# Optimization experiments

Measured on AMD Instinct MI355X. Metric: run time of the kernel, lower is better.

The kernel has to match this reference:

```python
import jax, jax.numpy as jnp
import numpy as np

B, NINP, NCLS = 16384, 2048, 100


def setup_inputs() -> dict:
    key = jax.random.key(0)
    k1, k2, k3, k4, k5 = jax.random.split(key, 5)
    s = 1.0 / np.sqrt(NINP)
    return {
        "time_series": jax.random.normal(k1, (B, NINP), jnp.float32),
        "w_weight": jax.random.uniform(k2, (NINP, NINP), jnp.float32, -s, s),
        "w_bias": jax.random.uniform(k3, (NINP,), jnp.float32, -s, s),
        "fc_weight": jax.random.uniform(k4, (NCLS, NINP), jnp.float32, -s, s),
        "fc_bias": jax.random.uniform(k5, (NCLS,), jnp.float32, -s, s),
    }


def reference(time_series, w_weight, w_bias, fc_weight, fc_bias):
    # time_series: [B, N]
    n = time_series.shape[1]
    # gamma = cumsum(softmax(w(x), axis=1), axis=1): monotone warp in (0, 1]
    gamma = jnp.cumsum(jax.nn.softmax(time_series @ w_weight.T + w_bias, axis=1), axis=1)
    # Interp1d(linspace(0,1,N), x, gamma): per-row linear interpolation,
    # sampling each series at the warped time points gamma.
    xs = jnp.linspace(0.0, 1.0, n, dtype=time_series.dtype)  # shared knot grid
    warped = jax.vmap(lambda g, y: jnp.interp(g, xs, y))(gamma, time_series)  # [B, N]
    return warped @ fc_weight.T + fc_bias  # [B, nclasses]
```

## Files before the change

kernel.cpp:

```cpp
#include <hip/hip_runtime.h>
#include <hip/hip_bf16.h>

#define BROWS 16384
#define NDIM  2048
#define NCLS  100

typedef __attribute__((ext_vector_type(8))) __bf16 bf16x8;
typedef __attribute__((ext_vector_type(4))) float f32x4;
typedef __attribute__((ext_vector_type(16))) float f32x16;
typedef __attribute__((ext_vector_type(4))) unsigned short u16x4;
typedef __attribute__((ext_vector_type(8))) unsigned short u16x8;

__device__ __forceinline__ unsigned short f2bf(float f) {
    union { float f; unsigned int u; } v; v.f = f;
    unsigned int u = v.u;
    unsigned int r = (u + 0x7fffu + ((u >> 16) & 1u)) >> 16;
    return (unsigned short)r;
}
__device__ __forceinline__ float bf2f(unsigned short h) {
    union { unsigned int u; float f; } v; v.u = ((unsigned int)h) << 16;
    return v.f;
}

#define GLOAD_LDS(g, l) \
    __builtin_amdgcn_global_load_lds((const __attribute__((address_space(1))) void*)(g), \
                                     (__attribute__((address_space(3))) void*)(l), 16, 0, 0)

__global__ __launch_bounds__(256) void prep_kernel(const float4* __restrict__ x,
                                                   const float4* __restrict__ w,
                                                   u16x4* __restrict__ xhi, u16x4* __restrict__ xlo,
                                                   u16x4* __restrict__ whi, u16x4* __restrict__ wlo,
                                                   int n4x, int n4w)
{
    int i = blockIdx.x * 256 + threadIdx.x;
    const float4* src; u16x4 *hi, *lo; int idx;
    if (i < n4x) { src = x; hi = xhi; lo = xlo; idx = i; }
    else { idx = i - n4x; if (idx >= n4w) return; src = w; hi = whi; lo = wlo; }
    float4 v = src[idx];
    u16x4 h, l;
    h.x = f2bf(v.x); l.x = f2bf(v.x - bf2f(h.x));
    h.y = f2bf(v.y); l.y = f2bf(v.y - bf2f(h.y));
    h.z = f2bf(v.z); l.z = f2bf(v.z - bf2f(h.z));
    h.w = f2bf(v.w); l.w = f2bf(v.w - bf2f(h.w));
    hi[idx] = h; lo[idx] = l;
}

__global__ __launch_bounds__(256) void cvt_bf16_kernel(const float4* __restrict__ src,
                                                       u16x4* __restrict__ dst, int n4)
{
    int i = blockIdx.x * 256 + threadIdx.x;
    if (i >= n4) return;
    float4 v = src[i];
    u16x4 h;
    h.x = f2bf(v.x); h.y = f2bf(v.y); h.z = f2bf(v.z); h.w = f2bf(v.w);
    dst[i] = h;
}

__global__ __launch_bounds__(256) void gemm1_mfma_fused_kernel(
        const unsigned short* __restrict__ xhi,
        const unsigned short* __restrict__ xlo,
        const unsigned short* __restrict__ whi,
        const unsigned short* __restrict__ wlo,
        const float* __restrict__ bias,
        float* __restrict__ C)
{
    __shared__ unsigned short sAh[128 * 32];
    __shared__ unsigned short sAl[128 * 32];
    __shared__ unsigned short sBh[128 * 32];
    __shared__ unsigned short sBl[128 * 32];

    const int tid  = threadIdx.x;
    const int lane = tid & 63;
    const int w    = tid >> 6;
    const int wm   = w & 1;
    const int wn   = w >> 1;
    const int m0   = blockIdx.y * 128;
    const int n0   = blockIdx.x * 128;

    const int c0 = w * 128 + lane;
    const int r0 = c0 >> 2;
    const int q0 = (c0 & 3) ^ ((r0 >> 1) & 3);
    const int c1 = c0 + 64;
    const int r1 = c1 >> 2;
    const int q1 = (c1 & 3) ^ ((r1 >> 1) & 3);

    const size_t a_goff0 = (size_t)(m0 + r0) * NDIM + q0 * 8;
    const size_t a_goff1 = (size_t)(m0 + r1) * NDIM + q1 * 8;
    const size_t b_goff0 = (size_t)(n0 + r0) * NDIM + q0 * 8;
    const size_t b_goff1 = (size_t)(n0 + r1) * NDIM + q1 * 8;

    unsigned short* ldsAh0 = &sAh[w * 1024];   unsigned short* ldsAh1 = &sAh[w * 1024 + 512];
    unsigned short* ldsAl0 = &sAl[w * 1024];   unsigned short* ldsAl1 = &sAl[w * 1024 + 512];
    unsigned short* ldsBh0 = &sBh[w * 1024];   unsigned short* ldsBh1 = &sBh[w * 1024 + 512];
    unsigned short* ldsBl0 = &sBl[w * 1024];   unsigned short* ldsBl1 = &sBl[w * 1024 + 512];

    const int ln32 = lane & 31;
    const int lk2  = lane >> 5;
    int offA[2][2], offB[2][2];
#pragma unroll
    for (int i = 0; i < 2; i++) {
#pragma unroll
        for (int ks = 0; ks < 2; ks++) {
            int ra = wm * 64 + i * 32 + ln32;
            offA[i][ks] = ra * 32 + (((2 * ks + lk2) ^ ((ra >> 1) & 3)) * 8);
            int rb = wn * 64 + i * 32 + ln32;
            offB[i][ks] = rb * 32 + (((2 * ks + lk2) ^ ((rb >> 1) & 3)) * 8);
        }
    }

    f32x16 acc[2][2];
#pragma unroll
    for (int i = 0; i < 2; i++)
#pragma unroll
        for (int j = 0; j < 2; j++)
#pragma unroll
            for (int r = 0; r < 16; r++) acc[i][j][r] = 0.f;

    for (int kt = 0; kt < NDIM; kt += 32) {
        GLOAD_LDS(xhi + a_goff0 + kt, ldsAh0);
        GLOAD_LDS(xhi + a_goff1 + kt, ldsAh1);
        GLOAD_LDS(xlo + a_goff0 + kt, ldsAl0);
        GLOAD_LDS(xlo + a_goff1 + kt, ldsAl1);
        GLOAD_LDS(whi + b_goff0 + kt, ldsBh0);
        GLOAD_LDS(whi + b_goff1 + kt, ldsBh1);
        GLOAD_LDS(wlo + b_goff0 + kt, ldsBl0);
        GLOAD_LDS(wlo + b_goff1 + kt, ldsBl1);
        __syncthreads();

#pragma unroll
        for (int ks = 0; ks < 2; ks++) {
            bf16x8 ah[2], al[2], bh[2], bl[2];
#pragma unroll
            for (int i = 0; i < 2; i++) {
                ah[i] = *(const bf16x8*)&sAh[offA[i][ks]];
                al[i] = *(const bf16x8*)&sAl[offA[i][ks]];
                bh[i] = *(const bf16x8*)&sBh[offB[i][ks]];
                bl[i] = *(const bf16x8*)&sBl[offB[i][ks]];
            }
#pragma unroll
            for (int i = 0; i < 2; i++)
#pragma unroll
                for (int j = 0; j < 2; j++) {
                    acc[i][j] = __builtin_amdgcn_mfma_f32_32x32x16_bf16(ah[i], bh[j], acc[i][j], 0, 0, 0);
                    acc[i][j] = __builtin_amdgcn_mfma_f32_32x32x16_bf16(ah[i], bl[j], acc[i][j], 0, 0, 0);
                    acc[i][j] = __builtin_amdgcn_mfma_f32_32x32x16_bf16(al[i], bh[j], acc[i][j], 0, 0, 0);
                }
        }
        __syncthreads();
    }

    float bb[2];
#pragma unroll
    for (int j = 0; j < 2; j++) bb[j] = bias[n0 + wn * 64 + j * 32 + ln32];
#pragma unroll
    for (int i = 0; i < 2; i++) {
#pragma unroll
        for (int j = 0; j < 2; j++) {
            const int n = n0 + wn * 64 + j * 32 + ln32;
#pragma unroll
            for (int reg = 0; reg < 16; reg++) {
                const int m = m0 + wm * 64 + i * 32 + (reg & 3) + 8 * (reg >> 2) + 4 * lk2;
                C[(size_t)m * NDIM + n] = acc[i][j][reg] + bb[j];
            }
        }
    }
}

#define SXI(i) ((i) + ((i) >> 5))

__global__ __launch_bounds__(256) void warp_bf16_kernel(const unsigned short* __restrict__ Xhi,
                                                        const unsigned short* __restrict__ Xlo,
                                                        const float* __restrict__ L,
                                                        unsigned short* __restrict__ Wout)
{
    const int N = NDIM;
    const int row = blockIdx.x;
    const int tid = threadIdx.x;
    const int lane = tid & 63;
    const int wave = tid >> 6;

    __shared__ float s_x[NDIM + NDIM / 32];
    __shared__ float s_red[4];
    __shared__ float s_wsum[4];

    const float* lrow = L + (size_t)row * N;

    float v[8];
    {
        float4 l0 = *(const float4*)(lrow + tid * 8);
        float4 l1 = *(const float4*)(lrow + tid * 8 + 4);
        v[0] = l0.x; v[1] = l0.y; v[2] = l0.z; v[3] = l0.w;
        v[4] = l1.x; v[5] = l1.y; v[6] = l1.z; v[7] = l1.w;
        u16x8 hx = *(const u16x8*)(Xhi + (size_t)row * N + tid * 8);
        u16x8 lx = *(const u16x8*)(Xlo + (size_t)row * N + tid * 8);
        float xv[8];
#pragma unroll
        for (int j = 0; j < 8; j++) xv[j] = bf2f(hx[j]) + bf2f(lx[j]);
        const int sb = SXI(tid * 8);
        *(float4*)&s_x[sb]     = make_float4(xv[0], xv[1], xv[2], xv[3]);
        *(float4*)&s_x[sb + 4] = make_float4(xv[4], xv[5], xv[6], xv[7]);
    }

    float mx = v[0];
#pragma unroll
    for (int j = 1; j < 8; j++) mx = fmaxf(mx, v[j]);
#pragma unroll
    for (int off = 32; off > 0; off >>= 1) mx = fmaxf(mx, __shfl_down(mx, off));
    if (lane == 0) s_red[wave] = mx;
    __syncthreads();
    mx = fmaxf(fmaxf(s_red[0], s_red[1]), fmaxf(s_red[2], s_red[3]));

    float c = 0.0f;
#pragma unroll
    for (int j = 0; j < 8; j++) {
        float e = __expf(v[j] - mx);
        c += e;
        v[j] = c;
    }

    float sc = c;
#pragma unroll
    for (int off = 1; off < 64; off <<= 1) {
        float t = __shfl_up(sc, off);
        if (lane >= off) sc += t;
    }
    if (lane == 63) s_wsum[wave] = sc;
    __syncthreads();
    float base = 0.0f, total = 0.0f;
#pragma unroll
    for (int w = 0; w < 4; w++) {
        float t = s_wsum[w];
        if (w < wave) base += t;
        total += t;
    }
    const float inv = 1.0f / total;
    const float prefix = base + (sc - c);

    u16x8 o;
#pragma unroll
    for (int j = 0; j < 8; j++) {
        float g = (prefix + v[j]) * inv;
        float pos = g * (float)(N - 1);
        pos = fminf(fmaxf(pos, 0.0f), (float)(N - 1));
        int i = (int)pos;
        if (i > N - 2) i = N - 2;
        float f = pos - (float)i;
        float x0 = s_x[SXI(i)];
        float x1 = s_x[SXI(i + 1)];
        o[j] = f2bf(fmaf(f, x1 - x0, x0));
    }
    *(u16x8*)(Wout + (size_t)row * N + tid * 8) = o;
}

__global__ __launch_bounds__(256) void gemm2_mfma_kernel(
        const unsigned short* __restrict__ Wp,
        const unsigned short* __restrict__ F,
        const float* __restrict__ fb,
        float* __restrict__ out)
{
    __shared__ unsigned short sA[64 * 64];
    __shared__ unsigned short sB[128 * 64];

    const int tid  = threadIdx.x;
    const int lane = tid & 63;
    const int w    = tid >> 6;
    const int wm   = w & 1;
    const int wn   = w >> 1;
    const int m0   = blockIdx.x * 64;

    size_t a_goff[2]; int a_lb[2];
#pragma unroll
    for (int t = 0; t < 2; t++) {
        const int c = t * 256 + tid;
        const int r = c >> 3, q = c & 7;
        a_goff[t] = (size_t)(m0 + r) * NDIM + ((q ^ (r & 7)) * 8);
        a_lb[t]   = (t * 256 + w * 64) * 8;
    }
    size_t b_goff[4]; int b_lb[4];
#pragma unroll
    for (int t = 0; t < 4; t++) {
        const int c = t * 256 + tid;
        const int r = c >> 3, q = c & 7;
        b_goff[t] = (size_t)(r < NCLS ? r : NCLS - 1) * NDIM + ((q ^ (r & 7)) * 8);
        b_lb[t]   = (t * 256 + w * 64) * 8;
    }

    const int lm = lane & 15;
    const int lk = lane >> 4;
    int offA[2][2], offB[4][2];
#pragma unroll
    for (int i = 0; i < 2; i++)
#pragma unroll
        for (int ks = 0; ks < 2; ks++) {
            const int r = wm * 32 + i * 16 + lm;
            offA[i][ks] = (r * 8 + ((ks * 4 + lk) ^ (r & 7))) * 8;
        }
#pragma unroll
    for (int j = 0; j < 4; j++)
#pragma unroll
        for (int ks = 0; ks < 2; ks++) {
            const int r = wn * 64 + j * 16 + lm;
            offB[j][ks] = (r * 8 + ((ks * 4 + lk) ^ (r & 7))) * 8;
        }

    f32x4 acc[2][4];
#pragma unroll
    for (int i = 0; i < 2; i++)
#pragma unroll
        for (int j = 0; j < 4; j++) acc[i][j] = (f32x4){0.f, 0.f, 0.f, 0.f};

    for (int kt = 0; kt < NDIM; kt += 64) {
#pragma unroll
        for (int t = 0; t < 2; t++) GLOAD_LDS(Wp + a_goff[t] + kt, &sA[a_lb[t]]);
#pragma unroll
        for (int t = 0; t < 4; t++) GLOAD_LDS(F + b_goff[t] + kt, &sB[b_lb[t]]);
        __syncthreads();

#pragma unroll
        for (int ks = 0; ks < 2; ks++) {
            bf16x8 af[2], bf[4];
#pragma unroll
            for (int i = 0; i < 2; i++) af[i] = *(const bf16x8*)&sA[offA[i][ks]];
#pragma unroll
            for (int j = 0; j < 4; j++) bf[j] = *(const bf16x8*)&sB[offB[j][ks]];
#pragma unroll
            for (int i = 0; i < 2; i++)
#pragma unroll
                for (int j = 0; j < 4; j++)
                    acc[i][j] = __builtin_amdgcn_mfma_f32_16x16x32_bf16(af[i], bf[j], acc[i][j], 0, 0, 0);
        }
        __syncthreads();
    }

    const int cn = lane & 15;
    const int rg = lane >> 4;
#pragma unroll
    for (int i = 0; i < 2; i++) {
#pragma unroll
        for (int j = 0; j < 4; j++) {
            const int n = wn * 64 + j * 16 + cn;
            if (n < NCLS) {
                const float bbn = fb[n];
#pragma unroll
                for (int reg = 0; reg < 4; reg++) {
                    const int m = m0 + wm * 32 + i * 16 + rg * 4 + reg;
                    out[(size_t)m * NCLS + n] = acc[i][j][reg] + bbn;
                }
            }
        }
    }
}

__global__ __launch_bounds__(256) void gemm1_kernel(const float* __restrict__ X,
                                                    const float* __restrict__ W,
                                                    const float* __restrict__ bias,
                                                    float* __restrict__ C)
{
    const int K = NDIM;
    __shared__ float sA[16][128];
    __shared__ float sB[16][128];
    const int tid = threadIdx.x;
    const int tx = tid & 15;
    const int ty = tid >> 4;
    const int m0 = blockIdx.y * 128;
    const int n0 = blockIdx.x * 128;
    float acc[8][8];
#pragma unroll
    for (int i = 0; i < 8; i++)
#pragma unroll
        for (int j = 0; j < 8; j++) acc[i][j] = 0.0f;
    const int s_m = tid >> 1;
    const int s_c = (tid & 1) * 8;
    const float* Ag = X + (size_t)(m0 + s_m) * K + s_c;
    const float* Bg = W + (size_t)(n0 + s_m) * K + s_c;
    for (int kt = 0; kt < K; kt += 16) {
        float4 av0 = *(const float4*)(Ag + kt);
        float4 av1 = *(const float4*)(Ag + kt + 4);
        float4 bv0 = *(const float4*)(Bg + kt);
        float4 bv1 = *(const float4*)(Bg + kt + 4);
        __syncthreads();
        sA[s_c + 0][s_m] = av0.x; sA[s_c + 1][s_m] = av0.y;
        sA[s_c + 2][s_m] = av0.z; sA[s_c + 3][s_m] = av0.w;
        sA[s_c + 4][s_m] = av1.x; sA[s_c + 5][s_m] = av1.y;
        sA[s_c + 6][s_m] = av1.z; sA[s_c + 7][s_m] = av1.w;
        sB[s_c + 0][s_m] = bv0.x; sB[s_c + 1][s_m] = bv0.y;
        sB[s_c + 2][s_m] = bv0.z; sB[s_c + 3][s_m] = bv0.w;
        sB[s_c + 4][s_m] = bv1.x; sB[s_c + 5][s_m] = bv1.y;
        sB[s_c + 6][s_m] = bv1.z; sB[s_c + 7][s_m] = bv1.w;
        __syncthreads();
#pragma unroll
        for (int k = 0; k < 16; k++) {
            float4 a0 = *(const float4*)&sA[k][ty * 8];
            float4 a1 = *(const float4*)&sA[k][ty * 8 + 4];
            float4 b0 = *(const float4*)&sB[k][tx * 8];
            float4 b1 = *(const float4*)&sB[k][tx * 8 + 4];
            float a[8] = {a0.x, a0.y, a0.z, a0.w, a1.x, a1.y, a1.z, a1.w};
            float b[8] = {b0.x, b0.y, b0.z, b0.w, b1.x, b1.y, b1.z, b1.w};
#pragma unroll
            for (int i = 0; i < 8; i++)
#pragma unroll
                for (int j = 0; j < 8; j++)
                    acc[i][j] = fmaf(a[i], b[j], acc[i][j]);
        }
    }
    float bb[8];
#pragma unroll
    for (int j = 0; j < 8; j++) bb[j] = bias[n0 + tx * 8 + j];
#pragma unroll
    for (int i = 0; i < 8; i++) {
        const int m = m0 + ty * 8 + i;
        float* crow = C + (size_t)m * NDIM + n0 + tx * 8;
        *(float4*)(crow)     = make_float4(acc[i][0] + bb[0], acc[i][1] + bb[1],
                                           acc[i][2] + bb[2], acc[i][3] + bb[3]);
        *(float4*)(crow + 4) = make_float4(acc[i][4] + bb[4], acc[i][5] + bb[5],
                                           acc[i][6] + bb[6], acc[i][7] + bb[7]);
    }
}

__global__ __launch_bounds__(256) void warp_kernel_f32(const float* __restrict__ X,
                                                       float* __restrict__ L)
{
    const int N = NDIM;
    const int row = blockIdx.x;
    const int tid = threadIdx.x;
    const int lane = tid & 63;
    const int wave = tid >> 6;
    __shared__ float s_x[NDIM];
    __shared__ float s_red[4];
    __shared__ float s_wsum[4];
    float* lrow = L + (size_t)row * N;
    const float* xrow = X + (size_t)row * N;
    float v[8];
    {
        float4 l0 = *(const float4*)(lrow + tid * 8);
        float4 l1 = *(const float4*)(lrow + tid * 8 + 4);
        v[0] = l0.x; v[1] = l0.y; v[2] = l0.z; v[3] = l0.w;
        v[4] = l1.x; v[5] = l1.y; v[6] = l1.z; v[7] = l1.w;
        float4 x0 = *(const float4*)(xrow + tid * 8);
        float4 x1 = *(const float4*)(xrow + tid * 8 + 4);
        *(float4*)&s_x[tid * 8]     = x0;
        *(float4*)&s_x[tid * 8 + 4] = x1;
    }
    float mx = v[0];
#pragma unroll
    for (int j = 1; j < 8; j++) mx = fmaxf(mx, v[j]);
#pragma unroll
    for (int off = 32; off > 0; off >>= 1) mx = fmaxf(mx, __shfl_down(mx, off));
    if (lane == 0) s_red[wave] = mx;
    __syncthreads();
    mx = fmaxf(fmaxf(s_red[0], s_red[1]), fmaxf(s_red[2], s_red[3]));
    float c = 0.0f;
#pragma unroll
    for (int j = 0; j < 8; j++) {
        float e = __expf(v[j] - mx);
        c += e;
        v[j] = c;
    }
    float sc = c;
#pragma unroll
    for (int off = 1; off < 64; off <<= 1) {
        float t = __shfl_up(sc, off);
        if (lane >= off) sc += t;
    }
    if (lane == 63) s_wsum[wave] = sc;
    __syncthreads();
    float base = 0.0f, total = 0.0f;
#pragma unroll
    for (int w = 0; w < 4; w++) {
        float t = s_wsum[w];
        if (w < wave) base += t;
        total += t;
    }
    const float inv = 1.0f / total;
    const float prefix = base + (sc - c);
    float w8[8];
#pragma unroll
    for (int j = 0; j < 8; j++) {
        float g = (prefix + v[j]) * inv;
        float pos = g * (float)(N - 1);
        pos = fminf(fmaxf(pos, 0.0f), (float)(N - 1));
        int i = (int)pos;
        if (i > N - 2) i = N - 2;
        float f = pos - (float)i;
        w8[j] = fmaf(f, s_x[i + 1] - s_x[i], s_x[i]);
    }
    *(float4*)(lrow + tid * 8)     = make_float4(w8[0], w8[1], w8[2], w8[3]);
    *(float4*)(lrow + tid * 8 + 4) = make_float4(w8[4], w8[5], w8[6], w8[7]);
}

__global__ __launch_bounds__(256) void gemm2_kernel(const float* __restrict__ Wp,
                                                    const float* __restrict__ F,
                                                    const float* __restrict__ fb,
                                                    float* __restrict__ out)
{
    const int K = NDIM;
    __shared__ float sA[16][64];
    __shared__ float sB[16][128];
    const int tid = threadIdx.x;
    const int tx = tid & 15;
    const int ty = tid >> 4;
    const int m0 = blockIdx.x * 64;
    float acc[4][8];
#pragma unroll
    for (int i = 0; i < 4; i++)
#pragma unroll
        for (int j = 0; j < 8; j++) acc[i][j] = 0.0f;
    const int a_m = tid >> 2;
    const int a_c = (tid & 3) * 4;
    const int b_n = tid >> 1;
    const int b_c = (tid & 1) * 8;
    const bool bvalid = (b_n < NCLS);
    const float* Ag = Wp + (size_t)(m0 + a_m) * K + a_c;
    const float* Bg = F + (size_t)b_n * K + b_c;
    for (int kt = 0; kt < K; kt += 16) {
        float4 av = *(const float4*)(Ag + kt);
        float4 bv0 = make_float4(0.f, 0.f, 0.f, 0.f);
        float4 bv1 = make_float4(0.f, 0.f, 0.f, 0.f);
        if (bvalid) {
            bv0 = *(const float4*)(Bg + kt);
            bv1 = *(const float4*)(Bg + kt + 4);
        }
        __syncthreads();
        sA[a_c + 0][a_m] = av.x; sA[a_c + 1][a_m] = av.y;
        sA[a_c + 2][a_m] = av.z; sA[a_c + 3][a_m] = av.w;
        sB[b_c + 0][b_n] = bv0.x; sB[b_c + 1][b_n] = bv0.y;
        sB[b_c + 2][b_n] = bv0.z; sB[b_c + 3][b_n] = bv0.w;
        sB[b_c + 4][b_n] = bv1.x; sB[b_c + 5][b_n] = bv1.y;
        sB[b_c + 6][b_n] = bv1.z; sB[b_c + 7][b_n] = bv1.w;
        __syncthreads();
#pragma unroll
        for (int k = 0; k < 16; k++) {
            float4 a4 = *(const float4*)&sA[k][ty * 4];
            float4 b0 = *(const float4*)&sB[k][tx * 8];
            float4 b1 = *(const float4*)&sB[k][tx * 8 + 4];
            float a[4] = {a4.x, a4.y, a4.z, a4.w};
            float b[8] = {b0.x, b0.y, b0.z, b0.w, b1.x, b1.y, b1.z, b1.w};
#pragma unroll
            for (int i = 0; i < 4; i++)
#pragma unroll
                for (int j = 0; j < 8; j++)
                    acc[i][j] = fmaf(a[i], b[j], acc[i][j]);
        }
    }
#pragma unroll
    for (int i = 0; i < 4; i++) {
        const int m = m0 + ty * 4 + i;
#pragma unroll
        for (int j = 0; j < 8; j++) {
            const int n = tx * 8 + j;
            if (n < NCLS) out[(size_t)m * NCLS + n] = acc[i][j] + fb[n];
        }
    }
}

extern "C" void kernel_launch(void* const* d_in, const int* in_sizes, int n_in,
                              void* d_out, int out_size, void* d_ws, size_t ws_size,
                              hipStream_t stream) {
    const float* x  = (const float*)d_in[0];
    const float* ww = (const float*)d_in[1];
    const float* wb = (const float*)d_in[2];
    const float* fw = (const float*)d_in[3];
    const float* fb = (const float*)d_in[4];
    float* out = (float*)d_out;

    char* ws = (char*)d_ws;
    float* logits = (float*)ws;
    const size_t LOGITS_B = (size_t)BROWS * NDIM * 4;
    const size_t XBF_B    = (size_t)BROWS * NDIM * 2;
    const size_t WBF_B    = (size_t)NDIM * NDIM * 2;
    unsigned short* xhi = (unsigned short*)(ws + LOGITS_B);
    unsigned short* xlo = (unsigned short*)(ws + LOGITS_B + XBF_B);
    unsigned short* whi = (unsigned short*)(ws + LOGITS_B + 2 * XBF_B);
    unsigned short* wlo = (unsigned short*)(ws + LOGITS_B + 2 * XBF_B + WBF_B);
    unsigned short* wbf = xlo;
    unsigned short* fwb = wlo;
    const size_t WS_NEED = LOGITS_B + 2 * XBF_B + 2 * WBF_B;

    if (ws_size >= WS_NEED) {
        const int n4x = BROWS * NDIM / 4;
        const int n4w = NDIM * NDIM / 4;
        prep_kernel<<<(n4x + n4w + 255) / 256, 256, 0, stream>>>(
            (const float4*)x, (const float4*)ww,
            (u16x4*)xhi, (u16x4*)xlo, (u16x4*)whi, (u16x4*)wlo, n4x, n4w);
        gemm1_mfma_fused_kernel<<<dim3(NDIM / 128, BROWS / 128), 256, 0, stream>>>(
            xhi, xlo, whi, wlo, wb, logits);
        warp_bf16_kernel<<<BROWS, 256, 0, stream>>>(xhi, xlo, logits, wbf);
        cvt_bf16_kernel<<<(NCLS * NDIM / 4 + 255) / 256, 256, 0, stream>>>(
            (const float4*)fw, (u16x4*)fwb, NCLS * NDIM / 4);
        gemm2_mfma_kernel<<<BROWS / 64, 256, 0, stream>>>(wbf, fwb, fb, out);
    } else {
        gemm1_kernel<<<dim3(NDIM / 128, BROWS / 128), 256, 0, stream>>>(x, ww, wb, logits);
        warp_kernel_f32<<<BROWS, 256, 0, stream>>>(x, logits);
        gemm2_kernel<<<BROWS / 64, 256, 0, stream>>>(logits, fw, fb, out);
    }
}
```

Measured before the change: 695.9 us.

## Double-buffer LDS tiles in both MFMA GEMM kernels to overlap loads

Both GEMM kernels now keep two LDS buffers. The main loop issues the async global-to-LDS load for the next K tile before computing on the current one, and is unrolled two tiles per iteration with one barrier per tile. The aim is to hide global-load latency behind MFMA work instead of stalling on every tile. In exchange, LDS per block doubles (64 KB in the split-bf16 GEMM), which can reduce the number of resident blocks per CU.

```diff
diff --git a/kernel.cpp b/kernel.cpp
--- a/kernel.cpp
+++ b/kernel.cpp
@@ -64,10 +64,10 @@
         const float* __restrict__ bias,
         float* __restrict__ C)
 {
-    __shared__ unsigned short sAh[128 * 32];
-    __shared__ unsigned short sAl[128 * 32];
-    __shared__ unsigned short sBh[128 * 32];
-    __shared__ unsigned short sBl[128 * 32];
+    __shared__ unsigned short sAh[2 * 128 * 32];
+    __shared__ unsigned short sAl[2 * 128 * 32];
+    __shared__ unsigned short sBh[2 * 128 * 32];
+    __shared__ unsigned short sBl[2 * 128 * 32];
 
     const int tid  = threadIdx.x;
     const int lane = tid & 63;
@@ -89,10 +89,8 @@
     const size_t b_goff0 = (size_t)(n0 + r0) * NDIM + q0 * 8;
     const size_t b_goff1 = (size_t)(n0 + r1) * NDIM + q1 * 8;
 
-    unsigned short* ldsAh0 = &sAh[w * 1024];   unsigned short* ldsAh1 = &sAh[w * 1024 + 512];
-    unsigned short* ldsAl0 = &sAl[w * 1024];   unsigned short* ldsAl1 = &sAl[w * 1024 + 512];
-    unsigned short* ldsBh0 = &sBh[w * 1024];   unsigned short* ldsBh1 = &sBh[w * 1024 + 512];
-    unsigned short* ldsBl0 = &sBl[w * 1024];   unsigned short* ldsBl1 = &sBl[w * 1024 + 512];
+    const int lb0 = w * 1024;
+    const int lb1 = w * 1024 + 512;
 
     const int ln32 = lane & 31;
     const int lk2  = lane >> 5;
@@ -116,38 +114,52 @@
 #pragma unroll
             for (int r = 0; r < 16; r++) acc[i][j][r] = 0.f;
 
-    for (int kt = 0; kt < NDIM; kt += 32) {
-        GLOAD_LDS(xhi + a_goff0 + kt, ldsAh0);
-        GLOAD_LDS(xhi + a_goff1 + kt, ldsAh1);
-        GLOAD_LDS(xlo + a_goff0 + kt, ldsAl0);
-        GLOAD_LDS(xlo + a_goff1 + kt, ldsAl1);
-        GLOAD_LDS(whi + b_goff0 + kt, ldsBh0);
-        GLOAD_LDS(whi + b_goff1 + kt, ldsBh1);
-        GLOAD_LDS(wlo + b_goff0 + kt, ldsBl0);
-        GLOAD_LDS(wlo + b_goff1 + kt, ldsBl1);
-        __syncthreads();
-
-#pragma unroll
-        for (int ks = 0; ks < 2; ks++) {
-            bf16x8 ah[2], al[2], bh[2], bl[2];
-#pragma unroll
-            for (int i = 0; i < 2; i++) {
-                ah[i] = *(const bf16x8*)&sAh[offA[i][ks]];
-                al[i] = *(const bf16x8*)&sAl[offA[i][ks]];
-                bh[i] = *(const bf16x8*)&sBh[offB[i][ks]];
-                bl[i] = *(const bf16x8*)&sBl[offB[i][ks]];
-            }
-#pragma unroll
-            for (int i = 0; i < 2; i++)
-#pragma unroll
-                for (int j = 0; j < 2; j++) {
-                    acc[i][j] = __builtin_amdgcn_mfma_f32_32x32x16_bf16(ah[i], bh[j], acc[i][j], 0, 0, 0);
-                    acc[i][j] = __builtin_amdgcn_mfma_f32_32x32x16_bf16(ah[i], bl[j], acc[i][j], 0, 0, 0);
-                    acc[i][j] = __builtin_amdgcn_mfma_f32_32x32x16_bf16(al[i], bh[j], acc[i][j], 0, 0, 0);
-                }
-        }
-        __syncthreads();
-    }
+#define G1_STAGE(B, KT) do { \
+    GLOAD_LDS(xhi + a_goff0 + (KT), &sAh[(B) * 4096 + lb0]); \
+    GLOAD_LDS(xhi + a_goff1 + (KT), &sAh[(B) * 4096 + lb1]); \
+    GLOAD_LDS(xlo + a_goff0 + (KT), &sAl[(B) * 4096 + lb0]); \
+    GLOAD_LDS(xlo + a_goff1 + (KT), &sAl[(B) * 4096 + lb1]); \
+    GLOAD_LDS(whi + b_goff0 + (KT), &sBh[(B) * 4096 + lb0]); \
+    GLOAD_LDS(whi + b_goff1 + (KT), &sBh[(B) * 4096 + lb1]); \
+    GLOAD_LDS(wlo + b_goff0 + (KT), &sBl[(B) * 4096 + lb0]); \
+    GLOAD_LDS(wlo + b_goff1 + (KT), &sBl[(B) * 4096 + lb1]); \
+} while (0)
+
+#define G1_COMPUTE(B) do { \
+    _Pragma("unroll") \
+    for (int ks = 0; ks < 2; ks++) { \
+        bf16x8 ah[2], al[2], bh[2], bl[2]; \
+        _Pragma("unroll") \
+        for (int i = 0; i < 2; i++) { \
+            ah[i] = *(const bf16x8*)&sAh[(B) * 4096 + offA[i][ks]]; \
+            al[i] = *(const bf16x8*)&sAl[(B) * 4096 + offA[i][ks]]; \
+            bh[i] = *(const bf16x8*)&sBh[(B) * 4096 + offB[i][ks]]; \
+            bl[i] = *(const bf16x8*)&sBl[(B) * 4096 + offB[i][ks]]; \
+        } \
+        _Pragma("unroll") \
+        for (int i = 0; i < 2; i++) \
+            _Pragma("unroll") \
+            for (int j = 0; j < 2; j++) { \
+                acc[i][j] = __builtin_amdgcn_mfma_f32_32x32x16_bf16(ah[i], bh[j], acc[i][j], 0, 0, 0); \
+                acc[i][j] = __builtin_amdgcn_mfma_f32_32x32x16_bf16(ah[i], bl[j], acc[i][j], 0, 0, 0); \
+                acc[i][j] = __builtin_amdgcn_mfma_f32_32x32x16_bf16(al[i], bh[j], acc[i][j], 0, 0, 0); \
+            } \
+    } \
+} while (0)
+
+    G1_STAGE(0, 0);
+
+    for (int kt = 0; kt < NDIM; kt += 64) {
+        __syncthreads();
+        G1_STAGE(1, kt + 32);
+        G1_COMPUTE(0);
+        __syncthreads();
+        if (kt + 64 < NDIM) G1_STAGE(0, kt + 64);
+        G1_COMPUTE(1);
+    }
+
+#undef G1_STAGE
+#undef G1_COMPUTE
 
     float bb[2];
 #pragma unroll
@@ -258,8 +270,8 @@
         const float* __restrict__ fb,
         float* __restrict__ out)
 {
-    __shared__ unsigned short sA[64 * 64];
-    __shared__ unsigned short sB[128 * 64];
+    __shared__ unsigned short sA[2 * 64 * 64];
+    __shared__ unsigned short sB[2 * 128 * 64];
 
     const int tid  = threadIdx.x;
     const int lane = tid & 63;
@@ -309,28 +321,42 @@
 #pragma unroll
         for (int j = 0; j < 4; j++) acc[i][j] = (f32x4){0.f, 0.f, 0.f, 0.f};
 
-    for (int kt = 0; kt < NDIM; kt += 64) {
-#pragma unroll
-        for (int t = 0; t < 2; t++) GLOAD_LDS(Wp + a_goff[t] + kt, &sA[a_lb[t]]);
-#pragma unroll
-        for (int t = 0; t < 4; t++) GLOAD_LDS(F + b_goff[t] + kt, &sB[b_lb[t]]);
-        __syncthreads();
-
-#pragma unroll
-        for (int ks = 0; ks < 2; ks++) {
-            bf16x8 af[2], bf[4];
-#pragma unroll
-            for (int i = 0; i < 2; i++) af[i] = *(const bf16x8*)&sA[offA[i][ks]];
-#pragma unroll
-            for (int j = 0; j < 4; j++) bf[j] = *(const bf16x8*)&sB[offB[j][ks]];
-#pragma unroll
-            for (int i = 0; i < 2; i++)
-#pragma unroll
-                for (int j = 0; j < 4; j++)
-                    acc[i][j] = __builtin_amdgcn_mfma_f32_16x16x32_bf16(af[i], bf[j], acc[i][j], 0, 0, 0);
-        }
-        __syncthreads();
-    }
+#define G2_STAGE(B, KT) do { \
+    _Pragma("unroll") \
+    for (int t = 0; t < 2; t++) GLOAD_LDS(Wp + a_goff[t] + (KT), &sA[(B) * 4096 + a_lb[t]]); \
+    _Pragma("unroll") \
+    for (int t = 0; t < 4; t++) GLOAD_LDS(F + b_goff[t] + (KT), &sB[(B) * 8192 + b_lb[t]]); \
+} while (0)
+
+#define G2_COMPUTE(B) do { \
+    _Pragma("unroll") \
+    for (int ks = 0; ks < 2; ks++) { \
+        bf16x8 af[2], bfr[4]; \
+        _Pragma("unroll") \
+        for (int i = 0; i < 2; i++) af[i] = *(const bf16x8*)&sA[(B) * 4096 + offA[i][ks]]; \
+        _Pragma("unroll") \
+        for (int j = 0; j < 4; j++) bfr[j] = *(const bf16x8*)&sB[(B) * 8192 + offB[j][ks]]; \
+        _Pragma("unroll") \
+        for (int i = 0; i < 2; i++) \
+            _Pragma("unroll") \
+            for (int j = 0; j < 4; j++) \
+                acc[i][j] = __builtin_amdgcn_mfma_f32_16x16x32_bf16(af[i], bfr[j], acc[i][j], 0, 0, 0); \
+    } \
+} while (0)
+
+    G2_STAGE(0, 0);
+
+    for (int kt = 0; kt < NDIM; kt += 128) {
+        __syncthreads();
+        G2_STAGE(1, kt + 64);
+        G2_COMPUTE(0);
+        __syncthreads();
+        if (kt + 128 < NDIM) G2_STAGE(0, kt + 128);
+        G2_COMPUTE(1);
+    }
+
+#undef G2_STAGE
+#undef G2_COMPUTE
 
     const int cn = lane & 15;
     const int rg = lane >> 4;
```

After: 723.0 us. +3.9%, slower.

## Widen gemm1 N-tile to 256 and double-buffer gemm2 LDS loads

Applied to the files above, without the earlier changes.

The split-bf16 logits GEMM now gives each block a 128x256 output tile, so each wave holds 2x4 32x32 accumulators and every loaded A fragment feeds twice as many MFMAs. This cuts redundant global and LDS traffic for the A operands, at the cost of more accumulator registers and therefore possibly lower occupancy. The classifier GEMM gets a two-stage LDS ping-pong: the next K-slice is issued with global_load_lds before the current one is computed, gated by explicit vmcnt waits and raw barriers. That overlaps load latency with MFMA work but doubles gemm2's LDS use, and the final iteration issues a dummy reload of slice 0 that is never consumed.

```diff
diff --git a/kernel.cpp b/kernel.cpp
--- a/kernel.cpp
+++ b/kernel.cpp
@@ -25,6 +25,9 @@
 #define GLOAD_LDS(g, l) \
     __builtin_amdgcn_global_load_lds((const __attribute__((address_space(1))) void*)(g), \
                                      (__attribute__((address_space(3))) void*)(l), 16, 0, 0)
+
+#define WAITCNT_VM(N) asm volatile("s_waitcnt vmcnt(" #N ")" ::: "memory")
+#define RAW_BARRIER() __builtin_amdgcn_s_barrier()
 
 __global__ __launch_bounds__(256) void prep_kernel(const float4* __restrict__ x,
                                                    const float4* __restrict__ w,
@@ -66,8 +69,8 @@
 {
     __shared__ unsigned short sAh[128 * 32];
     __shared__ unsigned short sAl[128 * 32];
-    __shared__ unsigned short sBh[128 * 32];
-    __shared__ unsigned short sBl[128 * 32];
+    __shared__ unsigned short sBh[256 * 32];
+    __shared__ unsigned short sBl[256 * 32];
 
     const int tid  = threadIdx.x;
     const int lane = tid & 63;
@@ -75,88 +78,105 @@
     const int wm   = w & 1;
     const int wn   = w >> 1;
     const int m0   = blockIdx.y * 128;
-    const int n0   = blockIdx.x * 128;
-
-    const int c0 = w * 128 + lane;
-    const int r0 = c0 >> 2;
-    const int q0 = (c0 & 3) ^ ((r0 >> 1) & 3);
-    const int c1 = c0 + 64;
-    const int r1 = c1 >> 2;
-    const int q1 = (c1 & 3) ^ ((r1 >> 1) & 3);
-
-    const size_t a_goff0 = (size_t)(m0 + r0) * NDIM + q0 * 8;
-    const size_t a_goff1 = (size_t)(m0 + r1) * NDIM + q1 * 8;
-    const size_t b_goff0 = (size_t)(n0 + r0) * NDIM + q0 * 8;
-    const size_t b_goff1 = (size_t)(n0 + r1) * NDIM + q1 * 8;
-
-    unsigned short* ldsAh0 = &sAh[w * 1024];   unsigned short* ldsAh1 = &sAh[w * 1024 + 512];
-    unsigned short* ldsAl0 = &sAl[w * 1024];   unsigned short* ldsAl1 = &sAl[w * 1024 + 512];
-    unsigned short* ldsBh0 = &sBh[w * 1024];   unsigned short* ldsBh1 = &sBh[w * 1024 + 512];
-    unsigned short* ldsBl0 = &sBl[w * 1024];   unsigned short* ldsBl1 = &sBl[w * 1024 + 512];
+    const int n0   = blockIdx.x * 256;
+
+    const int ca0 = w * 128 + lane;
+    const int ra0 = ca0 >> 2;
+    const int qa0 = (ca0 & 3) ^ ((ra0 >> 1) & 3);
+    const int ca1 = ca0 + 64;
+    const int ra1 = ca1 >> 2;
+    const int qa1 = (ca1 & 3) ^ ((ra1 >> 1) & 3);
+    const size_t a_goff0 = (size_t)(m0 + ra0) * NDIM + qa0 * 8;
+    const size_t a_goff1 = (size_t)(m0 + ra1) * NDIM + qa1 * 8;
+    const int a_lb0 = w * 1024;
+    const int a_lb1 = w * 1024 + 512;
+
+    size_t b_goff[4]; int b_lb[4];
+#pragma unroll
+    for (int t = 0; t < 4; t++) {
+        const int c = t * 256 + w * 64 + lane;
+        const int r = c >> 2;
+        const int q = (c & 3) ^ ((r >> 1) & 3);
+        b_goff[t] = (size_t)(n0 + r) * NDIM + q * 8;
+        b_lb[t]   = (t * 256 + w * 64) * 8;
+    }
 
     const int ln32 = lane & 31;
     const int lk2  = lane >> 5;
-    int offA[2][2], offB[2][2];
-#pragma unroll
-    for (int i = 0; i < 2; i++) {
+    int offA[2][2], offB[4][2];
+#pragma unroll
+    for (int i = 0; i < 2; i++)
 #pragma unroll
         for (int ks = 0; ks < 2; ks++) {
-            int ra = wm * 64 + i * 32 + ln32;
+            const int ra = wm * 64 + i * 32 + ln32;
             offA[i][ks] = ra * 32 + (((2 * ks + lk2) ^ ((ra >> 1) & 3)) * 8);
-            int rb = wn * 64 + i * 32 + ln32;
-            offB[i][ks] = rb * 32 + (((2 * ks + lk2) ^ ((rb >> 1) & 3)) * 8);
-        }
-    }
-
-    f32x16 acc[2][2];
+        }
+#pragma unroll
+    for (int j = 0; j < 4; j++)
+#pragma unroll
+        for (int ks = 0; ks < 2; ks++) {
+            const int rb = wn * 128 + j * 32 + ln32;
+            offB[j][ks] = rb * 32 + (((2 * ks + lk2) ^ ((rb >> 1) & 3)) * 8);
+        }
+
+    f32x16 acc[2][4];
 #pragma unroll
     for (int i = 0; i < 2; i++)
 #pragma unroll
-        for (int j = 0; j < 2; j++)
+        for (int j = 0; j < 4; j++)
 #pragma unroll
             for (int r = 0; r < 16; r++) acc[i][j][r] = 0.f;
 
     for (int kt = 0; kt < NDIM; kt += 32) {
-        GLOAD_LDS(xhi + a_goff0 + kt, ldsAh0);
-        GLOAD_LDS(xhi + a_goff1 + kt, ldsAh1);
-        GLOAD_LDS(xlo + a_goff0 + kt, ldsAl0);
-        GLOAD_LDS(xlo + a_goff1 + kt, ldsAl1);
-        GLOAD_LDS(whi + b_goff0 + kt, ldsBh0);
-        GLOAD_LDS(whi + b_goff1 + kt, ldsBh1);
-        GLOAD_LDS(wlo + b_goff0 + kt, ldsBl0);
-        GLOAD_LDS(wlo + b_goff1 + kt, ldsBl1);
+        GLOAD_LDS(xhi + a_goff0 + kt, &sAh[a_lb0]);
+        GLOAD_LDS(xhi + a_goff1 + kt, &sAh[a_lb1]);
+        GLOAD_LDS(xlo + a_goff0 + kt, &sAl[a_lb0]);
+        GLOAD_LDS(xlo + a_goff1 + kt, &sAl[a_lb1]);
+#pragma unroll
+        for (int t = 0; t < 4; t++) {
+            GLOAD_LDS(whi + b_goff[t] + kt, &sBh[b_lb[t]]);
+            GLOAD_LDS(wlo + b_goff[t] + kt, &sBl[b_lb[t]]);
+        }
         __syncthreads();
 
 #pragma unroll
         for (int ks = 0; ks < 2; ks++) {
-            bf16x8 ah[2], al[2], bh[2], bl[2];
+            bf16x8 ah[2], al[2];
 #pragma unroll
             for (int i = 0; i < 2; i++) {
                 ah[i] = *(const bf16x8*)&sAh[offA[i][ks]];
                 al[i] = *(const bf16x8*)&sAl[offA[i][ks]];
-                bh[i] = *(const bf16x8*)&sBh[offB[i][ks]];
-                bl[i] = *(const bf16x8*)&sBl[offB[i][ks]];
             }
 #pragma unroll
-            for (int i = 0; i < 2; i++)
-#pragma unroll
-                for (int j = 0; j < 2; j++) {
-                    acc[i][j] = __builtin_amdgcn_mfma_f32_32x32x16_bf16(ah[i], bh[j], acc[i][j], 0, 0, 0);
-                    acc[i][j] = __builtin_amdgcn_mfma_f32_32x32x16_bf16(ah[i], bl[j], acc[i][j], 0, 0, 0);
-                    acc[i][j] = __builtin_amdgcn_mfma_f32_32x32x16_bf16(al[i], bh[j], acc[i][j], 0, 0, 0);
+            for (int jp = 0; jp < 2; jp++) {
+                bf16x8 bh[2], bl[2];
+#pragma unroll
+                for (int jj = 0; jj < 2; jj++) {
+                    bh[jj] = *(const bf16x8*)&sBh[offB[jp * 2 + jj][ks]];
+                    bl[jj] = *(const bf16x8*)&sBl[offB[jp * 2 + jj][ks]];
                 }
+#pragma unroll
+                for (int i = 0; i < 2; i++)
+#pragma unroll
+                    for (int jj = 0; jj < 2; jj++) {
+                        const int j = jp * 2 + jj;
+                        acc[i][j] = __builtin_amdgcn_mfma_f32_32x32x16_bf16(ah[i], bh[jj], acc[i][j], 0, 0, 0);
+                        acc[i][j] = __builtin_amdgcn_mfma_f32_32x32x16_bf16(ah[i], bl[jj], acc[i][j], 0, 0, 0);
+                        acc[i][j] = __builtin_amdgcn_mfma_f32_32x32x16_bf16(al[i], bh[jj], acc[i][j], 0, 0, 0);
+                    }
+            }
         }
         __syncthreads();
     }
 
-    float bb[2];
-#pragma unroll
-    for (int j = 0; j < 2; j++) bb[j] = bias[n0 + wn * 64 + j * 32 + ln32];
+    float bb[4];
+#pragma unroll
+    for (int j = 0; j < 4; j++) bb[j] = bias[n0 + wn * 128 + j * 32 + ln32];
 #pragma unroll
     for (int i = 0; i < 2; i++) {
 #pragma unroll
-        for (int j = 0; j < 2; j++) {
-            const int n = n0 + wn * 64 + j * 32 + ln32;
+        for (int j = 0; j < 4; j++) {
+            const int n = n0 + wn * 128 + j * 32 + ln32;
 #pragma unroll
             for (int reg = 0; reg < 16; reg++) {
                 const int m = m0 + wm * 64 + i * 32 + (reg & 3) + 8 * (reg >> 2) + 4 * lk2;
@@ -258,8 +278,8 @@
         const float* __restrict__ fb,
         float* __restrict__ out)
 {
-    __shared__ unsigned short sA[64 * 64];
-    __shared__ unsigned short sB[128 * 64];
+    __shared__ unsigned short sA[2 * 64 * 64];
+    __shared__ unsigned short sB[2 * 128 * 64];
 
     const int tid  = threadIdx.x;
     const int lane = tid & 63;
@@ -309,28 +329,46 @@
 #pragma unroll
         for (int j = 0; j < 4; j++) acc[i][j] = (f32x4){0.f, 0.f, 0.f, 0.f};
 
-    for (int kt = 0; kt < NDIM; kt += 64) {
-#pragma unroll
-        for (int t = 0; t < 2; t++) GLOAD_LDS(Wp + a_goff[t] + kt, &sA[a_lb[t]]);
-#pragma unroll
-        for (int t = 0; t < 4; t++) GLOAD_LDS(F + b_goff[t] + kt, &sB[b_lb[t]]);
-        __syncthreads();
-
-#pragma unroll
-        for (int ks = 0; ks < 2; ks++) {
-            bf16x8 af[2], bf[4];
-#pragma unroll
-            for (int i = 0; i < 2; i++) af[i] = *(const bf16x8*)&sA[offA[i][ks]];
-#pragma unroll
-            for (int j = 0; j < 4; j++) bf[j] = *(const bf16x8*)&sB[offB[j][ks]];
-#pragma unroll
-            for (int i = 0; i < 2; i++)
-#pragma unroll
-                for (int j = 0; j < 4; j++)
-                    acc[i][j] = __builtin_amdgcn_mfma_f32_16x16x32_bf16(af[i], bf[j], acc[i][j], 0, 0, 0);
-        }
-        __syncthreads();
-    }
+#define G2_STAGE(B, KT) do { \
+    _Pragma("unroll") \
+    for (int t = 0; t < 2; t++) GLOAD_LDS(Wp + a_goff[t] + (KT), &sA[(B) * 4096 + a_lb[t]]); \
+    _Pragma("unroll") \
+    for (int t = 0; t < 4; t++) GLOAD_LDS(F + b_goff[t] + (KT), &sB[(B) * 8192 + b_lb[t]]); \
+} while (0)
+
+#define G2_COMPUTE(B) do { \
+    _Pragma("unroll") \
+    for (int ks = 0; ks < 2; ks++) { \
+        bf16x8 af[2], bfr[4]; \
+        _Pragma("unroll") \
+        for (int i = 0; i < 2; i++) af[i] = *(const bf16x8*)&sA[(B) * 4096 + offA[i][ks]]; \
+        _Pragma("unroll") \
+        for (int j = 0; j < 4; j++) bfr[j] = *(const bf16x8*)&sB[(B) * 8192 + offB[j][ks]]; \
+        _Pragma("unroll") \
+        for (int i = 0; i < 2; i++) \
+            _Pragma("unroll") \
+            for (int j = 0; j < 4; j++) \
+                acc[i][j] = __builtin_amdgcn_mfma_f32_16x16x32_bf16(af[i], bfr[j], acc[i][j], 0, 0, 0); \
+    } \
+} while (0)
+
+    G2_STAGE(0, 0);
+
+    for (int kt = 0; kt < NDIM; kt += 128) {
+        G2_STAGE(1, kt + 64);
+        WAITCNT_VM(6);
+        RAW_BARRIER();
+        G2_COMPUTE(0);
+        RAW_BARRIER();
+        G2_STAGE(0, (kt + 128 < NDIM) ? kt + 128 : 0);
+        WAITCNT_VM(6);
+        RAW_BARRIER();
+        G2_COMPUTE(1);
+        RAW_BARRIER();
+    }
+
+#undef G2_STAGE
+#undef G2_COMPUTE
 
     const int cn = lane & 15;
     const int rg = lane >> 4;
@@ -582,7 +620,7 @@
         prep_kernel<<<(n4x + n4w + 255) / 256, 256, 0, stream>>>(
             (const float4*)x, (const float4*)ww,
             (u16x4*)xhi, (u16x4*)xlo, (u16x4*)whi, (u16x4*)wlo, n4x, n4w);
-        gemm1_mfma_fused_kernel<<<dim3(NDIM / 128, BROWS / 128), 256, 0, stream>>>(
+        gemm1_mfma_fused_kernel<<<dim3(NDIM / 256, BROWS / 128), 256, 0, stream>>>(
             xhi, xlo, whi, wlo, wb, logits);
         warp_bf16_kernel<<<BROWS, 256, 0, stream>>>(xhi, xlo, logits, wbf);
         cvt_bf16_kernel<<<(NCLS * NDIM / 4 + 255) / 256, 256, 0, stream>>>(
```

After: 857.7 us. 1.23x slower.
